# Optimization experiments

Measured on AMD Instinct MI355X. Metric: run time of the kernel, lower is better.

Reference implementation:

```python
import jax, jax.numpy as jnp
import numpy as np

B, NA, NB, DF, H, DO, NT = 32, 128, 1024, 128, 512, 128, 5
NPAIR = NT * NT  # nn_index = z1*5 + z2 -> 25 pair-type MLPs


def setup_inputs() -> dict:
    key = jax.random.key(0)
    ks = jax.random.split(key, 6)
    z = jax.random.randint(ks[0], (B, NA), 0, NT)
    r = jax.random.normal(ks[1], (B, NA, 3), jnp.float32) * 5.0
    x = jax.random.normal(ks[2], (B, NA, DF), jnp.float32)
    t = jax.random.randint(ks[3], (B, NB, 2), 0, NA)
    pad = NB // 8  # last 1/8 of bonds are -1 padding, as in the torch module
    t = t.at[:, NB - pad:, :].set(-1)
    # Stacked per-pair-type 2-layer MLP params (map_list)
    W1 = jax.random.normal(ks[4], (NPAIR, 2 * DF, H), jnp.float32) / np.sqrt(2.0 * DF)
    b1 = jnp.zeros((NPAIR, H), jnp.float32)
    W2 = jax.random.normal(ks[5], (NPAIR, H, DO), jnp.float32) / np.sqrt(1.0 * H)
    b2 = jnp.zeros((NPAIR, DO), jnp.float32)
    return dict(z=z, r=r, x=x, t=t, W1=W1, b1=b1, W2=W2, b2=b2)


def reference(z, r, x, t, W1, b1, W2, b2):
    n_batch, n_bonds, _ = t.shape
    n_atoms = x.shape[1]
    x_f = x.reshape(-1, x.shape[-1])          # [B*NA, DF]
    z_f = z.reshape(-1)                        # [B*NA]
    r_f = r.reshape(-1, 3)                     # [B*NA, 3]
    offs = (jnp.arange(n_batch) * n_atoms)[:, None, None]
    valid = t[:, :, 0] != -1                   # [B, NB]
    tg = jnp.clip(t, 0, None) + offs           # global atom indices (padding clamped to 0)
    t1 = tg[:, :, 0].reshape(-1)
    t2 = tg[:, :, 1].reshape(-1)
    vmask = valid.reshape(-1)                  # [N] = [B*NB]
    # gather+concat pair features; zero out padded rows (masked_scatter into zeros)
    x_c = jnp.concatenate([x_f[t1], x_f[t2]], axis=1) * vmask[:, None].astype(x.dtype)
    z1 = z_f[t1]
    z2 = z_f[t2]
    nn_index = jnp.where(vmask, z1 * NT + z2, -1)
    # per-pair-type MLP dispatch (loop over fixed 25 types; rows selected by mask)
    y = jnp.zeros((x_c.shape[0], W2.shape[-1]), x.dtype)
    for i in range(NPAIR):
        h = jax.nn.silu(x_c @ W1[i] + b1[i])
        out_i = h @ W2[i] + b2[i]
        y = jnp.where((nn_index == i)[:, None], out_i, y)
    y = y.reshape(n_batch, n_bonds, -1)
    # normalized bond vectors, zeroed for padded bonds
    v = (r_f[t2] - r_f[t1]).reshape(n_batch, n_bonds, 3)
    n2 = jnp.sum(v * v, axis=2, keepdims=True)
    v = v / jnp.sqrt(jnp.clip(n2, 1e-24, None))  # == clamp(norm, 1e-12)
    v = v * valid[:, :, None].astype(v.dtype)
    return (z, x, t, y, v)
```

## Files before the change

kernel.cpp:

```cpp
#include <hip/hip_runtime.h>
#include <cstddef>
#include <cstdint>

#define NBATCH 32
#define NATOM  128
#define DFEAT  128
#define HDIM   512
#define DOUT   128
#define NTYPE  5
#define NPAIR  25
#define NBOND  32768
#define CAP    1408
#define TPT    22
#define GBLK   550

#define OFF_X 4096
#define OFF_T 528384
#define OFF_Y 593920
#define OFF_V 4788224

#define PRE_A 580
#define PRE_B 256
#define PRE_C 1600
#define PRE_D 800
#define PRE_BLK (PRE_A+PRE_B+PRE_C+PRE_D)

typedef __attribute__((ext_vector_type(8))) short short8;
typedef __attribute__((ext_vector_type(4))) float f32x4;

#define GAS(x) ((__attribute__((address_space(1))) const void*)(x))
#define LAS(x) ((__attribute__((address_space(3))) void*)(x))

__device__ __forceinline__ unsigned short f2bf(float f) {
    unsigned u = __float_as_uint(f);
    u = (u + 0x7FFFu + ((u >> 16) & 1u)) >> 16;
    return (unsigned short)u;
}

__global__ __launch_bounds__(256) void k_pre(const int* __restrict__ z,
                                             const float* __restrict__ x,
                                             const int* __restrict__ t,
                                             const float* __restrict__ W1,
                                             const float* __restrict__ W2,
                                             float* __restrict__ out,
                                             short* __restrict__ x_bf,
                                             short* __restrict__ W1p,
                                             short* __restrict__ W2p,
                                             int* __restrict__ cursors) {
    int bid = blockIdx.x, tid = threadIdx.x;
    if (bid == 0 && tid < 32) cursors[tid] = 0;
    if (bid < PRE_A) {
        int i4 = (bid * 256 + tid) * 4;
        float4 o;
        if (i4 < OFF_X) {
            const int4 zi = *(const int4*)&z[i4];
            o = make_float4((float)zi.x, (float)zi.y, (float)zi.z, (float)zi.w);
        } else if (i4 < OFF_T) {
            o = *(const float4*)&x[i4 - OFF_X];
        } else {
            const int4 ti = *(const int4*)&t[i4 - OFF_T];
            o = make_float4((float)ti.x, (float)ti.y, (float)ti.z, (float)ti.w);
        }
        *(float4*)&out[i4] = o;
    } else if (bid < PRE_A + PRE_B) {
        int idx = (bid - PRE_A) * 256 + tid;
        const float4* px = (const float4*)&x[idx * 8];
        float4 fa = px[0], fb = px[1];
        short8 v;
        v[0]=(short)f2bf(fa.x); v[1]=(short)f2bf(fa.y); v[2]=(short)f2bf(fa.z); v[3]=(short)f2bf(fa.w);
        v[4]=(short)f2bf(fb.x); v[5]=(short)f2bf(fb.y); v[6]=(short)f2bf(fb.z); v[7]=(short)f2bf(fb.w);
        *((short8*)x_bf + idx) = v;
    } else if (bid < PRE_A + PRE_B + PRE_C) {
        int idx = (bid - PRE_A - PRE_B) * 256 + tid;
        int l  = idx & 63;
        int cf = (idx >> 6) & 31;
        int ks = (idx >> 11) & 7;
        int p  = idx >> 14;
        int col = cf*16 + (l & 15);
        int kb  = ks*32 + (l >> 4)*8;
        const float* src = W1 + ((size_t)p*2*DFEAT + kb)*HDIM + col;
        short8 v;
        #pragma unroll
        for (int j = 0; j < 8; ++j) v[j] = (short)f2bf(src[(size_t)j*HDIM]);
        *((short8*)W1p + idx) = v;
    } else {
        int idx = (bid - PRE_A - PRE_B - PRE_C) * 256 + tid;
        int l  = idx & 63;
        int cf = (idx >> 6) & 7;
        int ks = (idx >> 9) & 15;
        int p  = idx >> 13;
        int col = cf*16 + (l & 15);
        int kb  = ks*32 + (l >> 4)*8;
        const float* src = W2 + ((size_t)p*HDIM + kb)*DOUT + col;
        short8 v;
        #pragma unroll
        for (int j = 0; j < 8; ++j) v[j] = (short)f2bf(src[(size_t)j*DOUT]);
        *((short8*)W2p + idx) = v;
    }
}

__global__ __launch_bounds__(256) void k_scatter(const int* __restrict__ z,
                                                 const float* __restrict__ r,
                                                 const int* __restrict__ t,
                                                 float* __restrict__ out_v,
                                                 float* __restrict__ y_out,
                                                 int* __restrict__ cursors,
                                                 int* __restrict__ bond_ids) {
    __shared__ int hist[NPAIR];
    __shared__ int base[NPAIR];
    int tid = threadIdx.x;
    if (tid < NPAIR) hist[tid] = 0;
    __syncthreads();

    int i = blockIdx.x * 256 + tid;
    int b = i >> 10;
    int t1 = t[2*i], t2 = t[2*i+1];
    float vx = 0.f, vy = 0.f, vz = 0.f;
    int p = -1, rk = 0;
    if (t1 != -1) {
        int g1 = b*NATOM + t1, g2 = b*NATOM + t2;
        p = z[g1]*NTYPE + z[g2];
        rk = atomicAdd(&hist[p], 1);
        float dx = r[3*g2+0]-r[3*g1+0];
        float dy = r[3*g2+1]-r[3*g1+1];
        float dz = r[3*g2+2]-r[3*g1+2];
        float n2 = fmaxf(dx*dx+dy*dy+dz*dz, 1e-24f);
        float inv = 1.0f / sqrtf(n2);
        vx = dx*inv; vy = dy*inv; vz = dz*inv;
    } else {
        float4 zr = make_float4(0.f, 0.f, 0.f, 0.f);
        float4* yp = (float4*)&y_out[(size_t)i * DOUT];
        #pragma unroll
        for (int c = 0; c < DOUT/4; ++c) yp[c] = zr;
    }
    out_v[3*i+0] = vx; out_v[3*i+1] = vy; out_v[3*i+2] = vz;
    __syncthreads();
    if (tid < NPAIR) base[tid] = atomicAdd(&cursors[tid], hist[tid]);
    __syncthreads();
    if (p >= 0) {
        int pos = base[p] + rk;
        if (pos < CAP) bond_ids[p*CAP + pos] = i;
    }
}

#define STAGE(cc_, rr_) do { \
    int _c = (cc_), _r = (rr_); \
    if (_r >= 12) { _r -= 12; _c += 1; if (_c >= 4) _c = 0; } \
    const char* _s; \
    if (_r < 8) _s = (const char*)W1p + (((size_t)(p*8 + _r)*32 + _c*8 + wc*2)*64 + l)*16; \
    else        _s = (const char*)W2p + (((size_t)(p*16 + _c*4 + (_r-8))*8 + wc*2)*64 + l)*16; \
    char* _d = (char*)wbuf + ((rr_)%3)*8192 + wc*2048 + l*16; \
    __builtin_amdgcn_global_load_lds(GAS(_s), LAS(_d), 16, 0, 0); \
    __builtin_amdgcn_global_load_lds(GAS(_s+1024), LAS(_d+1024), 16, 0, 0); \
} while(0)

__global__ __launch_bounds__(256, 2) void k_gemm(const short* __restrict__ x_bf,
                                                 const int* __restrict__ t,
                                                 const short* __restrict__ W1p,
                                                 const float* __restrict__ b1,
                                                 const short* __restrict__ W2p,
                                                 const float* __restrict__ b2,
                                                 const int* __restrict__ cursors,
                                                 const int* __restrict__ bond_ids,
                                                 float* __restrict__ y_out) {
    int orig = blockIdx.x;
    int xcd = orig & 7, ib = orig >> 3;
    int wk = (xcd < 6 ? xcd*69 : 414 + (xcd-6)*68) + ib;
    int p = wk / TPT, tileIdx = wk % TPT;
    int cnt = min(cursors[p], CAP);
    if (tileIdx*64 >= cnt) return;
    int nb = min(64, cnt - tileIdx*64);
    int ntiles = (cnt + 63) >> 6;

    __shared__ short xs[64*256];
    __shared__ short hs[64*128];
    __shared__ char  wbuf[3*8192];
    __shared__ float b1s[HDIM];
    __shared__ float b2s[DOUT];
    __shared__ int   srow[64][2];
    __shared__ int   sb[64];

    int tid = threadIdx.x;
    int l = tid & 63, wc = tid >> 6;
    int lr = l & 15, lq = l >> 4;
    int klq = lq * 16;

    if (tid < 64) {
        int bi = (tid < nb) ? bond_ids[p*CAP + tileIdx*64 + tid] : -1;
        sb[tid] = bi;
        int r0 = 0, r1 = 0;
        if (bi >= 0) { int b = bi >> 10; r0 = b*NATOM + t[2*bi]; r1 = b*NATOM + t[2*bi+1]; }
        srow[tid][0] = r0; srow[tid][1] = r1;
    }

    {
        float snk = 0.f;
        const char* w1t = (const char*)W1p + (size_t)p*262144;
        int o1 = (int)(((long)tileIdx * 262144) / ntiles) & ~63;
        int e1 = (int)(((long)(tileIdx+1) * 262144) / ntiles);
        for (int o = o1 + tid*16; o < e1; o += 4096) {
            float4 v = *(const float4*)(w1t + o);
            snk += v.x + v.y + v.z + v.w;
        }
        const char* w2t = (const char*)W2p + (size_t)p*131072;
        int o2 = (int)(((long)tileIdx * 131072) / ntiles) & ~63;
        int e2 = (int)(((long)(tileIdx+1) * 131072) / ntiles);
        for (int o = o2 + tid*16; o < e2; o += 4096) {
            float4 v = *(const float4*)(w2t + o);
            snk += v.x + v.y + v.z + v.w;
        }
        asm volatile("" :: "v"(snk));
    }

    if (tid < 128)
        __builtin_amdgcn_global_load_lds(GAS((const char*)(b1 + (size_t)p*HDIM) + tid*16),
                                         LAS((char*)b1s + tid*16), 16, 0, 0);
    if (tid < 32)
        __builtin_amdgcn_global_load_lds(GAS((const char*)(b2 + (size_t)p*DOUT) + tid*16),
                                         LAS((char*)b2s + tid*16), 16, 0, 0);
    STAGE(0, 0);
    STAGE(0, 1);
    __syncthreads();

    #pragma unroll
    for (int j = 0; j < 8; ++j) {
        int o = j*4096 + tid*16;
        int row = o >> 9;
        int c16 = ((o >> 4) & 31) ^ (row & 7);
        const char* src = (const char*)x_bf + ((size_t)srow[row][c16 >> 4]*DFEAT + (c16 & 15)*8)*2;
        __builtin_amdgcn_global_load_lds(GAS(src), LAS((char*)xs + o), 16, 0, 0);
    }
    __syncthreads();

    f32x4 yacc[4][2] = {};

    for (int c = 0; c < 4; ++c) {
        float b1c0 = b1s[c*128 + wc*32 + lr];
        float b1c1 = b1s[c*128 + wc*32 + 16 + lr];
        f32x4 acc1[4][2] = {};
        #pragma unroll
        for (int r = 0; r < 8; ++r) {
            short8 a0, a1, a2, a3;
            {
                const char* xb = (const char*)xs;
                a0 = *(const short8*)(xb + (0*16+lr)*512 + ((r*64 + klq) ^ (((0*16+lr)&7) << 4)));
                a1 = *(const short8*)(xb + (1*16+lr)*512 + ((r*64 + klq) ^ (((1*16+lr)&7) << 4)));
                a2 = *(const short8*)(xb + (2*16+lr)*512 + ((r*64 + klq) ^ (((2*16+lr)&7) << 4)));
                a3 = *(const short8*)(xb + (3*16+lr)*512 + ((r*64 + klq) ^ (((3*16+lr)&7) << 4)));
            }
            STAGE(c, r + 2);
            asm volatile("s_waitcnt vmcnt(4)" ::: "memory");
            const char* wb = (const char*)wbuf + (r%3)*8192 + wc*2048 + l*16;
            short8 w0 = *(const short8*)wb;
            short8 w1 = *(const short8*)(wb + 1024);
            __builtin_amdgcn_s_setprio(1);
            acc1[0][0] = __builtin_amdgcn_mfma_f32_16x16x32_bf16(a0, w0, acc1[0][0], 0, 0, 0);
            acc1[0][1] = __builtin_amdgcn_mfma_f32_16x16x32_bf16(a0, w1, acc1[0][1], 0, 0, 0);
            acc1[1][0] = __builtin_amdgcn_mfma_f32_16x16x32_bf16(a1, w0, acc1[1][0], 0, 0, 0);
            acc1[1][1] = __builtin_amdgcn_mfma_f32_16x16x32_bf16(a1, w1, acc1[1][1], 0, 0, 0);
            acc1[2][0] = __builtin_amdgcn_mfma_f32_16x16x32_bf16(a2, w0, acc1[2][0], 0, 0, 0);
            acc1[2][1] = __builtin_amdgcn_mfma_f32_16x16x32_bf16(a2, w1, acc1[2][1], 0, 0, 0);
            acc1[3][0] = __builtin_amdgcn_mfma_f32_16x16x32_bf16(a3, w0, acc1[3][0], 0, 0, 0);
            acc1[3][1] = __builtin_amdgcn_mfma_f32_16x16x32_bf16(a3, w1, acc1[3][1], 0, 0, 0);
            __builtin_amdgcn_s_setprio(0);
        }
        #pragma unroll
        for (int rf = 0; rf < 4; ++rf) {
            #pragma unroll
            for (int cf = 0; cf < 2; ++cf) {
                int colb = (wc*32 + cf*16 + lr) * 2;
                float bb = cf ? b1c1 : b1c0;
                #pragma unroll
                for (int reg = 0; reg < 4; ++reg) {
                    int row = rf*16 + lq*4 + reg;
                    float sv = acc1[rf][cf][reg] + bb;
                    float hv = sv / (1.0f + __expf(-sv));
                    *(unsigned short*)((char*)hs + row*256 + (colb ^ ((row & 7) << 4))) = f2bf(hv);
                }
            }
        }
        asm volatile("s_waitcnt lgkmcnt(0)" ::: "memory");
        __builtin_amdgcn_s_barrier();

        #pragma unroll
        for (int r2 = 8; r2 < 12; ++r2) {
            short8 a0, a1, a2, a3;
            {
                const char* hb = (const char*)hs;
                int s2 = r2 - 8;
                a0 = *(const short8*)(hb + (0*16+lr)*256 + ((s2*64 + klq) ^ (((0*16+lr)&7) << 4)));
                a1 = *(const short8*)(hb + (1*16+lr)*256 + ((s2*64 + klq) ^ (((1*16+lr)&7) << 4)));
                a2 = *(const short8*)(hb + (2*16+lr)*256 + ((s2*64 + klq) ^ (((2*16+lr)&7) << 4)));
                a3 = *(const short8*)(hb + (3*16+lr)*256 + ((s2*64 + klq) ^ (((3*16+lr)&7) << 4)));
            }
            STAGE(c, r2 + 2);
            asm volatile("s_waitcnt vmcnt(4)" ::: "memory");
            const char* wb = (const char*)wbuf + (r2%3)*8192 + wc*2048 + l*16;
            short8 w0 = *(const short8*)wb;
            short8 w1 = *(const short8*)(wb + 1024);
            __builtin_amdgcn_s_setprio(1);
            yacc[0][0] = __builtin_amdgcn_mfma_f32_16x16x32_bf16(a0, w0, yacc[0][0], 0, 0, 0);
            yacc[0][1] = __builtin_amdgcn_mfma_f32_16x16x32_bf16(a0, w1, yacc[0][1], 0, 0, 0);
            yacc[1][0] = __builtin_amdgcn_mfma_f32_16x16x32_bf16(a1, w0, yacc[1][0], 0, 0, 0);
            yacc[1][1] = __builtin_amdgcn_mfma_f32_16x16x32_bf16(a1, w1, yacc[1][1], 0, 0, 0);
            yacc[2][0] = __builtin_amdgcn_mfma_f32_16x16x32_bf16(a2, w0, yacc[2][0], 0, 0, 0);
            yacc[2][1] = __builtin_amdgcn_mfma_f32_16x16x32_bf16(a2, w1, yacc[2][1], 0, 0, 0);
            yacc[3][0] = __builtin_amdgcn_mfma_f32_16x16x32_bf16(a3, w0, yacc[3][0], 0, 0, 0);
            yacc[3][1] = __builtin_amdgcn_mfma_f32_16x16x32_bf16(a3, w1, yacc[3][1], 0, 0, 0);
            __builtin_amdgcn_s_setprio(0);
        }
        if (c < 3) {
            asm volatile("s_waitcnt lgkmcnt(0)" ::: "memory");
            __builtin_amdgcn_s_barrier();
        }
    }

    float bo0 = b2s[wc*32 + lr], bo1 = b2s[wc*32 + 16 + lr];
    #pragma unroll
    for (int rf = 0; rf < 4; ++rf) {
        #pragma unroll
        for (int cf = 0; cf < 2; ++cf) {
            int col = wc*32 + cf*16 + lr;
            float bo = cf ? bo1 : bo0;
            #pragma unroll
            for (int reg = 0; reg < 4; ++reg) {
                int row = rf*16 + lq*4 + reg;
                if (row < nb)
                    y_out[(size_t)sb[row]*DOUT + col] = yacc[rf][cf][reg] + bo;
            }
        }
    }
}

extern "C" void kernel_launch(void* const* d_in, const int* in_sizes, int n_in,
                              void* d_out, int out_size, void* d_ws, size_t ws_size,
                              hipStream_t stream) {
    const int*   z  = (const int*)  d_in[0];
    const float* r  = (const float*)d_in[1];
    const float* x  = (const float*)d_in[2];
    const int*   t  = (const int*)  d_in[3];
    const float* W1 = (const float*)d_in[4];
    const float* b1 = (const float*)d_in[5];
    const float* W2 = (const float*)d_in[6];
    const float* b2 = (const float*)d_in[7];
    float* out = (float*)d_out;

    char* ws = (char*)d_ws;
    int*   cursors  = (int*)(ws);
    int*   bond_ids = (int*)(ws + 256);
    short* x_bf     = (short*)(ws + 141312);
    short* W1p      = (short*)(ws + 1189888);
    short* W2p      = (short*)(ws + 7743488);

    k_pre<<<PRE_BLK, 256, 0, stream>>>(z, x, t, W1, W2, out, x_bf, W1p, W2p, cursors);
    k_scatter<<<NBOND/256, 256, 0, stream>>>(z, r, t, out + OFF_V, out + OFF_Y, cursors, bond_ids);
    k_gemm<<<GBLK, 256, 0, stream>>>(x_bf, t, W1p, b1, W2p, b2, cursors, bond_ids, out + OFF_Y);
}
```

Measured before the change: 45.62 us.

## Merge scatter into prep kernel and software-pipeline GEMM fragment loads

Folds the bond scatter/histogram work into the preprocessing kernel, with cursors zeroed by a memset. This saves a kernel launch. The x→bf16 conversion now happens inside the copy branch, so x is read once. The GEMM inner loops prefetch the next step's LDS A and W fragments while the current MFMAs run, and wait on vmcnt(2) instead of vmcnt(4). SiLU uses v_rcp_f32 instead of a divide. The risks are higher register pressure, and a tighter vmcnt wait that may stall on the prefetch.

```diff
diff --git a/kernel.cpp b/kernel.cpp
--- a/kernel.cpp
+++ b/kernel.cpp
@@ -20,10 +20,10 @@
 #define OFF_V 4788224
 
 #define PRE_A 580
-#define PRE_B 256
 #define PRE_C 1600
 #define PRE_D 800
-#define PRE_BLK (PRE_A+PRE_B+PRE_C+PRE_D)
+#define SCAT  128
+#define PREP_BLK (PRE_A+PRE_C+PRE_D+SCAT)
 
 typedef __attribute__((ext_vector_type(8))) short short8;
 typedef __attribute__((ext_vector_type(4))) float f32x4;
@@ -37,18 +37,19 @@
     return (unsigned short)u;
 }
 
-__global__ __launch_bounds__(256) void k_pre(const int* __restrict__ z,
-                                             const float* __restrict__ x,
-                                             const int* __restrict__ t,
-                                             const float* __restrict__ W1,
-                                             const float* __restrict__ W2,
-                                             float* __restrict__ out,
-                                             short* __restrict__ x_bf,
-                                             short* __restrict__ W1p,
-                                             short* __restrict__ W2p,
-                                             int* __restrict__ cursors) {
+__global__ __launch_bounds__(256) void k_prep(const int* __restrict__ z,
+                                              const float* __restrict__ x,
+                                              const int* __restrict__ t,
+                                              const float* __restrict__ r,
+                                              const float* __restrict__ W1,
+                                              const float* __restrict__ W2,
+                                              float* __restrict__ out,
+                                              short* __restrict__ x_bf,
+                                              short* __restrict__ W1p,
+                                              short* __restrict__ W2p,
+                                              int* __restrict__ cursors,
+                                              int* __restrict__ bond_ids) {
     int bid = blockIdx.x, tid = threadIdx.x;
-    if (bid == 0 && tid < 32) cursors[tid] = 0;
     if (bid < PRE_A) {
         int i4 = (bid * 256 + tid) * 4;
         float4 o;
@@ -57,21 +58,17 @@
             o = make_float4((float)zi.x, (float)zi.y, (float)zi.z, (float)zi.w);
         } else if (i4 < OFF_T) {
             o = *(const float4*)&x[i4 - OFF_X];
+            short4 s4;
+            s4.x = (short)f2bf(o.x); s4.y = (short)f2bf(o.y);
+            s4.z = (short)f2bf(o.z); s4.w = (short)f2bf(o.w);
+            *(short4*)&x_bf[i4 - OFF_X] = s4;
         } else {
             const int4 ti = *(const int4*)&t[i4 - OFF_T];
             o = make_float4((float)ti.x, (float)ti.y, (float)ti.z, (float)ti.w);
         }
         *(float4*)&out[i4] = o;
-    } else if (bid < PRE_A + PRE_B) {
+    } else if (bid < PRE_A + PRE_C) {
         int idx = (bid - PRE_A) * 256 + tid;
-        const float4* px = (const float4*)&x[idx * 8];
-        float4 fa = px[0], fb = px[1];
-        short8 v;
-        v[0]=(short)f2bf(fa.x); v[1]=(short)f2bf(fa.y); v[2]=(short)f2bf(fa.z); v[3]=(short)f2bf(fa.w);
-        v[4]=(short)f2bf(fb.x); v[5]=(short)f2bf(fb.y); v[6]=(short)f2bf(fb.z); v[7]=(short)f2bf(fb.w);
-        *((short8*)x_bf + idx) = v;
-    } else if (bid < PRE_A + PRE_B + PRE_C) {
-        int idx = (bid - PRE_A - PRE_B) * 256 + tid;
         int l  = idx & 63;
         int cf = (idx >> 6) & 31;
         int ks = (idx >> 11) & 7;
@@ -83,8 +80,8 @@
         #pragma unroll
         for (int j = 0; j < 8; ++j) v[j] = (short)f2bf(src[(size_t)j*HDIM]);
         *((short8*)W1p + idx) = v;
-    } else {
-        int idx = (bid - PRE_A - PRE_B - PRE_C) * 256 + tid;
+    } else if (bid < PRE_A + PRE_C + PRE_D) {
+        int idx = (bid - PRE_A - PRE_C) * 256 + tid;
         int l  = idx & 63;
         int cf = (idx >> 6) & 7;
         int ks = (idx >> 9) & 15;
@@ -96,50 +93,41 @@
         #pragma unroll
         for (int j = 0; j < 8; ++j) v[j] = (short)f2bf(src[(size_t)j*DOUT]);
         *((short8*)W2p + idx) = v;
-    }
-}
-
-__global__ __launch_bounds__(256) void k_scatter(const int* __restrict__ z,
-                                                 const float* __restrict__ r,
-                                                 const int* __restrict__ t,
-                                                 float* __restrict__ out_v,
-                                                 float* __restrict__ y_out,
-                                                 int* __restrict__ cursors,
-                                                 int* __restrict__ bond_ids) {
-    __shared__ int hist[NPAIR];
-    __shared__ int base[NPAIR];
-    int tid = threadIdx.x;
-    if (tid < NPAIR) hist[tid] = 0;
-    __syncthreads();
-
-    int i = blockIdx.x * 256 + tid;
-    int b = i >> 10;
-    int t1 = t[2*i], t2 = t[2*i+1];
-    float vx = 0.f, vy = 0.f, vz = 0.f;
-    int p = -1, rk = 0;
-    if (t1 != -1) {
-        int g1 = b*NATOM + t1, g2 = b*NATOM + t2;
-        p = z[g1]*NTYPE + z[g2];
-        rk = atomicAdd(&hist[p], 1);
-        float dx = r[3*g2+0]-r[3*g1+0];
-        float dy = r[3*g2+1]-r[3*g1+1];
-        float dz = r[3*g2+2]-r[3*g1+2];
-        float n2 = fmaxf(dx*dx+dy*dy+dz*dz, 1e-24f);
-        float inv = 1.0f / sqrtf(n2);
-        vx = dx*inv; vy = dy*inv; vz = dz*inv;
     } else {
-        float4 zr = make_float4(0.f, 0.f, 0.f, 0.f);
-        float4* yp = (float4*)&y_out[(size_t)i * DOUT];
-        #pragma unroll
-        for (int c = 0; c < DOUT/4; ++c) yp[c] = zr;
-    }
-    out_v[3*i+0] = vx; out_v[3*i+1] = vy; out_v[3*i+2] = vz;
-    __syncthreads();
-    if (tid < NPAIR) base[tid] = atomicAdd(&cursors[tid], hist[tid]);
-    __syncthreads();
-    if (p >= 0) {
-        int pos = base[p] + rk;
-        if (pos < CAP) bond_ids[p*CAP + pos] = i;
+        __shared__ int hist[NPAIR];
+        __shared__ int base[NPAIR];
+        if (tid < NPAIR) hist[tid] = 0;
+        __syncthreads();
+        int i = (bid - PRE_A - PRE_C - PRE_D) * 256 + tid;
+        int b = i >> 10;
+        int t1 = t[2*i], t2 = t[2*i+1];
+        float vx = 0.f, vy = 0.f, vz = 0.f;
+        int p = -1, rk = 0;
+        if (t1 != -1) {
+            int g1 = b*NATOM + t1, g2 = b*NATOM + t2;
+            p = z[g1]*NTYPE + z[g2];
+            rk = atomicAdd(&hist[p], 1);
+            float dx = r[3*g2+0]-r[3*g1+0];
+            float dy = r[3*g2+1]-r[3*g1+1];
+            float dz = r[3*g2+2]-r[3*g1+2];
+            float n2 = fmaxf(dx*dx+dy*dy+dz*dz, 1e-24f);
+            float inv = 1.0f / sqrtf(n2);
+            vx = dx*inv; vy = dy*inv; vz = dz*inv;
+        } else {
+            float4 zr = make_float4(0.f, 0.f, 0.f, 0.f);
+            float4* yp = (float4*)&out[OFF_Y + (size_t)i * DOUT];
+            #pragma unroll
+            for (int c = 0; c < DOUT/4; ++c) yp[c] = zr;
+        }
+        float* out_v = out + OFF_V;
+        out_v[3*i+0] = vx; out_v[3*i+1] = vy; out_v[3*i+2] = vz;
+        __syncthreads();
+        if (tid < NPAIR) base[tid] = atomicAdd(&cursors[tid], hist[tid]);
+        __syncthreads();
+        if (p >= 0) {
+            int pos = base[p] + rk;
+            if (pos < CAP) bond_ids[p*CAP + pos] = i;
+        }
     }
 }
 
@@ -152,6 +140,28 @@
     char* _d = (char*)wbuf + ((rr_)%3)*8192 + wc*2048 + l*16; \
     __builtin_amdgcn_global_load_lds(GAS(_s), LAS(_d), 16, 0, 0); \
     __builtin_amdgcn_global_load_lds(GAS(_s+1024), LAS(_d+1024), 16, 0, 0); \
+} while(0)
+
+#define XFRAG(dst, rf_, step_) do { \
+    int _row = (rf_)*16 + lr; \
+    dst = *(const short8*)((const char*)xs + _row*512 + (((step_)*64 + klq) ^ ((_row & 7) << 4))); \
+} while(0)
+#define HFRAG(dst, rf_, step_) do { \
+    int _row = (rf_)*16 + lr; \
+    dst = *(const short8*)((const char*)hs + _row*256 + (((step_)*64 + klq) ^ ((_row & 7) << 4))); \
+} while(0)
+
+#define MFMA8(ACC) do { \
+    __builtin_amdgcn_s_setprio(1); \
+    ACC[0][0] = __builtin_amdgcn_mfma_f32_16x16x32_bf16(a0, w0, ACC[0][0], 0, 0, 0); \
+    ACC[0][1] = __builtin_amdgcn_mfma_f32_16x16x32_bf16(a0, w1, ACC[0][1], 0, 0, 0); \
+    ACC[1][0] = __builtin_amdgcn_mfma_f32_16x16x32_bf16(a1, w0, ACC[1][0], 0, 0, 0); \
+    ACC[1][1] = __builtin_amdgcn_mfma_f32_16x16x32_bf16(a1, w1, ACC[1][1], 0, 0, 0); \
+    ACC[2][0] = __builtin_amdgcn_mfma_f32_16x16x32_bf16(a2, w0, ACC[2][0], 0, 0, 0); \
+    ACC[2][1] = __builtin_amdgcn_mfma_f32_16x16x32_bf16(a2, w1, ACC[2][1], 0, 0, 0); \
+    ACC[3][0] = __builtin_amdgcn_mfma_f32_16x16x32_bf16(a3, w0, ACC[3][0], 0, 0, 0); \
+    ACC[3][1] = __builtin_amdgcn_mfma_f32_16x16x32_bf16(a3, w1, ACC[3][1], 0, 0, 0); \
+    __builtin_amdgcn_s_setprio(0); \
 } while(0)
 
 __global__ __launch_bounds__(256, 2) void k_gemm(const short* __restrict__ x_bf,
@@ -234,35 +244,30 @@
 
     f32x4 yacc[4][2] = {};
 
+    short8 a0, a1, a2, a3, w0, w1;
+    XFRAG(a0, 0, 0); XFRAG(a1, 1, 0); XFRAG(a2, 2, 0); XFRAG(a3, 3, 0);
+    {
+        const char* wb = (const char*)wbuf + wc*2048 + l*16;
+        w0 = *(const short8*)wb;
+        w1 = *(const short8*)(wb + 1024);
+    }
+
     for (int c = 0; c < 4; ++c) {
         float b1c0 = b1s[c*128 + wc*32 + lr];
         float b1c1 = b1s[c*128 + wc*32 + 16 + lr];
         f32x4 acc1[4][2] = {};
         #pragma unroll
-        for (int r = 0; r < 8; ++r) {
-            short8 a0, a1, a2, a3;
-            {
-                const char* xb = (const char*)xs;
-                a0 = *(const short8*)(xb + (0*16+lr)*512 + ((r*64 + klq) ^ (((0*16+lr)&7) << 4)));
-                a1 = *(const short8*)(xb + (1*16+lr)*512 + ((r*64 + klq) ^ (((1*16+lr)&7) << 4)));
-                a2 = *(const short8*)(xb + (2*16+lr)*512 + ((r*64 + klq) ^ (((2*16+lr)&7) << 4)));
-                a3 = *(const short8*)(xb + (3*16+lr)*512 + ((r*64 + klq) ^ (((3*16+lr)&7) << 4)));
-            }
-            STAGE(c, r + 2);
-            asm volatile("s_waitcnt vmcnt(4)" ::: "memory");
-            const char* wb = (const char*)wbuf + (r%3)*8192 + wc*2048 + l*16;
-            short8 w0 = *(const short8*)wb;
-            short8 w1 = *(const short8*)(wb + 1024);
-            __builtin_amdgcn_s_setprio(1);
-            acc1[0][0] = __builtin_amdgcn_mfma_f32_16x16x32_bf16(a0, w0, acc1[0][0], 0, 0, 0);
-            acc1[0][1] = __builtin_amdgcn_mfma_f32_16x16x32_bf16(a0, w1, acc1[0][1], 0, 0, 0);
-            acc1[1][0] = __builtin_amdgcn_mfma_f32_16x16x32_bf16(a1, w0, acc1[1][0], 0, 0, 0);
-            acc1[1][1] = __builtin_amdgcn_mfma_f32_16x16x32_bf16(a1, w1, acc1[1][1], 0, 0, 0);
-            acc1[2][0] = __builtin_amdgcn_mfma_f32_16x16x32_bf16(a2, w0, acc1[2][0], 0, 0, 0);
-            acc1[2][1] = __builtin_amdgcn_mfma_f32_16x16x32_bf16(a2, w1, acc1[2][1], 0, 0, 0);
-            acc1[3][0] = __builtin_amdgcn_mfma_f32_16x16x32_bf16(a3, w0, acc1[3][0], 0, 0, 0);
-            acc1[3][1] = __builtin_amdgcn_mfma_f32_16x16x32_bf16(a3, w1, acc1[3][1], 0, 0, 0);
-            __builtin_amdgcn_s_setprio(0);
+        for (int rr = 0; rr < 8; ++rr) {
+            short8 na0, na1, na2, na3;
+            if (rr < 7) { XFRAG(na0, 0, rr+1); XFRAG(na1, 1, rr+1); XFRAG(na2, 2, rr+1); XFRAG(na3, 3, rr+1); }
+            STAGE(c, rr + 2);
+            asm volatile("s_waitcnt vmcnt(2)" ::: "memory");
+            const char* nwb = (const char*)wbuf + ((rr+1)%3)*8192 + wc*2048 + l*16;
+            short8 nw0 = *(const short8*)nwb;
+            short8 nw1 = *(const short8*)(nwb + 1024);
+            MFMA8(acc1);
+            if (rr < 7) { a0 = na0; a1 = na1; a2 = na2; a3 = na3; }
+            w0 = nw0; w1 = nw1;
         }
         #pragma unroll
         for (int rf = 0; rf < 4; ++rf) {
@@ -274,40 +279,30 @@
                 for (int reg = 0; reg < 4; ++reg) {
                     int row = rf*16 + lq*4 + reg;
                     float sv = acc1[rf][cf][reg] + bb;
-                    float hv = sv / (1.0f + __expf(-sv));
-                    *(unsigned short*)((char*)hs + row*256 + (colb ^ ((row & 7) << 4))) = f2bf(hv);
+                    float den = 1.0f + __expf(-sv);
+                    float rc;
+                    asm("v_rcp_f32 %0, %1" : "=v"(rc) : "v"(den));
+                    *(unsigned short*)((char*)hs + row*256 + (colb ^ ((row & 7) << 4))) = f2bf(sv * rc);
                 }
             }
         }
         asm volatile("s_waitcnt lgkmcnt(0)" ::: "memory");
         __builtin_amdgcn_s_barrier();
 
-        #pragma unroll
-        for (int r2 = 8; r2 < 12; ++r2) {
-            short8 a0, a1, a2, a3;
-            {
-                const char* hb = (const char*)hs;
-                int s2 = r2 - 8;
-                a0 = *(const short8*)(hb + (0*16+lr)*256 + ((s2*64 + klq) ^ (((0*16+lr)&7) << 4)));
-                a1 = *(const short8*)(hb + (1*16+lr)*256 + ((s2*64 + klq) ^ (((1*16+lr)&7) << 4)));
-                a2 = *(const short8*)(hb + (2*16+lr)*256 + ((s2*64 + klq) ^ (((2*16+lr)&7) << 4)));
-                a3 = *(const short8*)(hb + (3*16+lr)*256 + ((s2*64 + klq) ^ (((3*16+lr)&7) << 4)));
-            }
-            STAGE(c, r2 + 2);
-            asm volatile("s_waitcnt vmcnt(4)" ::: "memory");
-            const char* wb = (const char*)wbuf + (r2%3)*8192 + wc*2048 + l*16;
-            short8 w0 = *(const short8*)wb;
-            short8 w1 = *(const short8*)(wb + 1024);
-            __builtin_amdgcn_s_setprio(1);
-            yacc[0][0] = __builtin_amdgcn_mfma_f32_16x16x32_bf16(a0, w0, yacc[0][0], 0, 0, 0);
-            yacc[0][1] = __builtin_amdgcn_mfma_f32_16x16x32_bf16(a0, w1, yacc[0][1], 0, 0, 0);
-            yacc[1][0] = __builtin_amdgcn_mfma_f32_16x16x32_bf16(a1, w0, yacc[1][0], 0, 0, 0);
-            yacc[1][1] = __builtin_amdgcn_mfma_f32_16x16x32_bf16(a1, w1, yacc[1][1], 0, 0, 0);
-            yacc[2][0] = __builtin_amdgcn_mfma_f32_16x16x32_bf16(a2, w0, yacc[2][0], 0, 0, 0);
-            yacc[2][1] = __builtin_amdgcn_mfma_f32_16x16x32_bf16(a2, w1, yacc[2][1], 0, 0, 0);
-            yacc[3][0] = __builtin_amdgcn_mfma_f32_16x16x32_bf16(a3, w0, yacc[3][0], 0, 0, 0);
-            yacc[3][1] = __builtin_amdgcn_mfma_f32_16x16x32_bf16(a3, w1, yacc[3][1], 0, 0, 0);
-            __builtin_amdgcn_s_setprio(0);
+        HFRAG(a0, 0, 0); HFRAG(a1, 1, 0); HFRAG(a2, 2, 0); HFRAG(a3, 3, 0);
+        #pragma unroll
+        for (int r2 = 0; r2 < 4; ++r2) {
+            short8 na0, na1, na2, na3;
+            if (r2 < 3) { HFRAG(na0, 0, r2+1); HFRAG(na1, 1, r2+1); HFRAG(na2, 2, r2+1); HFRAG(na3, 3, r2+1); }
+            else        { XFRAG(na0, 0, 0);    XFRAG(na1, 1, 0);    XFRAG(na2, 2, 0);    XFRAG(na3, 3, 0);    }
+            STAGE(c, r2 + 10);
+            asm volatile("s_waitcnt vmcnt(2)" ::: "memory");
+            const char* nwb = (const char*)wbuf + ((r2+9)%3)*8192 + wc*2048 + l*16;
+            short8 nw0 = *(const short8*)nwb;
+            short8 nw1 = *(const short8*)(nwb + 1024);
+            MFMA8(yacc);
+            a0 = na0; a1 = na1; a2 = na2; a3 = na3;
+            w0 = nw0; w1 = nw1;
         }
         if (c < 3) {
             asm volatile("s_waitcnt lgkmcnt(0)" ::: "memory");
@@ -352,7 +347,7 @@
     short* W1p      = (short*)(ws + 1189888);
     short* W2p      = (short*)(ws + 7743488);
 
-    k_pre<<<PRE_BLK, 256, 0, stream>>>(z, x, t, W1, W2, out, x_bf, W1p, W2p, cursors);
-    k_scatter<<<NBOND/256, 256, 0, stream>>>(z, r, t, out + OFF_V, out + OFF_Y, cursors, bond_ids);
+    hipMemsetAsync(cursors, 0, 128, stream);
+    k_prep<<<PREP_BLK, 256, 0, stream>>>(z, x, t, r, W1, W2, out, x_bf, W1p, W2p, cursors, bond_ids);
     k_gemm<<<GBLK, 256, 0, stream>>>(x_bf, t, W1p, b1, W2p, b2, cursors, bond_ids, out + OFF_Y);
 }
```

Result: slower. 48.67 us (+6.7%).

## Fuse scatter into prep kernel and interleave W1/W2 packing per stage

Applied to the files above, without the earlier changes.

Merges the bond-scatter kernel into the preprocessing kernel, with cursor reset done by a memset, and folds the x bf16 conversion into the output-copy blocks. It packs W1 and W2 into one stage-ordered buffer so each GEMM stage loads a contiguous 8KB chunk, and gathers x rows directly from bond_ids without the srow staging barrier. It also removes setprio hints and uses a fast reciprocal in SiLU. The aim is to cut launch count, address arithmetic and one sync, at the cost of an extra memset and a larger prep kernel in which scatter blocks run alongside packing blocks.

```diff
diff --git a/kernel.cpp b/kernel.cpp
--- a/kernel.cpp
+++ b/kernel.cpp
@@ -20,10 +20,9 @@
 #define OFF_V 4788224
 
 #define PRE_A 580
-#define PRE_B 256
-#define PRE_C 1600
-#define PRE_D 800
-#define PRE_BLK (PRE_A+PRE_B+PRE_C+PRE_D)
+#define PACKB 2400
+#define SCAT  128
+#define PRE_BLK (PRE_A+PACKB+SCAT)
 
 typedef __attribute__((ext_vector_type(8))) short short8;
 typedef __attribute__((ext_vector_type(4))) float f32x4;
@@ -40,15 +39,15 @@
 __global__ __launch_bounds__(256) void k_pre(const int* __restrict__ z,
                                              const float* __restrict__ x,
                                              const int* __restrict__ t,
+                                             const float* __restrict__ r,
                                              const float* __restrict__ W1,
                                              const float* __restrict__ W2,
                                              float* __restrict__ out,
                                              short* __restrict__ x_bf,
-                                             short* __restrict__ W1p,
-                                             short* __restrict__ W2p,
-                                             int* __restrict__ cursors) {
+                                             short* __restrict__ Wpk,
+                                             int* __restrict__ cursors,
+                                             int* __restrict__ bond_ids) {
     int bid = blockIdx.x, tid = threadIdx.x;
-    if (bid == 0 && tid < 32) cursors[tid] = 0;
     if (bid < PRE_A) {
         int i4 = (bid * 256 + tid) * 4;
         float4 o;
@@ -57,108 +56,90 @@
             o = make_float4((float)zi.x, (float)zi.y, (float)zi.z, (float)zi.w);
         } else if (i4 < OFF_T) {
             o = *(const float4*)&x[i4 - OFF_X];
+            short4 s4;
+            s4.x = (short)f2bf(o.x); s4.y = (short)f2bf(o.y);
+            s4.z = (short)f2bf(o.z); s4.w = (short)f2bf(o.w);
+            *(short4*)&x_bf[i4 - OFF_X] = s4;
         } else {
             const int4 ti = *(const int4*)&t[i4 - OFF_T];
             o = make_float4((float)ti.x, (float)ti.y, (float)ti.z, (float)ti.w);
         }
         *(float4*)&out[i4] = o;
-    } else if (bid < PRE_A + PRE_B) {
+    } else if (bid < PRE_A + PACKB) {
         int idx = (bid - PRE_A) * 256 + tid;
-        const float4* px = (const float4*)&x[idx * 8];
-        float4 fa = px[0], fb = px[1];
+        int l   = idx & 63;
+        int u   = (idx >> 6) & 1;
+        int wcp = (idx >> 7) & 3;
+        int q   = idx >> 9;
+        int p   = q / 48;
+        int s   = q - p*48;
+        int c   = s / 12;
+        int rr  = s - c*12;
+        int lr = l & 15, kb = (l >> 4)*8;
         short8 v;
-        v[0]=(short)f2bf(fa.x); v[1]=(short)f2bf(fa.y); v[2]=(short)f2bf(fa.z); v[3]=(short)f2bf(fa.w);
-        v[4]=(short)f2bf(fb.x); v[5]=(short)f2bf(fb.y); v[6]=(short)f2bf(fb.z); v[7]=(short)f2bf(fb.w);
-        *((short8*)x_bf + idx) = v;
-    } else if (bid < PRE_A + PRE_B + PRE_C) {
-        int idx = (bid - PRE_A - PRE_B) * 256 + tid;
-        int l  = idx & 63;
-        int cf = (idx >> 6) & 31;
-        int ks = (idx >> 11) & 7;
-        int p  = idx >> 14;
-        int col = cf*16 + (l & 15);
-        int kb  = ks*32 + (l >> 4)*8;
-        const float* src = W1 + ((size_t)p*2*DFEAT + kb)*HDIM + col;
-        short8 v;
-        #pragma unroll
-        for (int j = 0; j < 8; ++j) v[j] = (short)f2bf(src[(size_t)j*HDIM]);
-        *((short8*)W1p + idx) = v;
+        if (rr < 8) {
+            int col = (c*8 + wcp*2 + u)*16 + lr;
+            const float* src = W1 + ((size_t)p*256 + rr*32 + kb)*HDIM + col;
+            #pragma unroll
+            for (int j = 0; j < 8; ++j) v[j] = (short)f2bf(src[(size_t)j*HDIM]);
+        } else {
+            int col = (wcp*2 + u)*16 + lr;
+            const float* src = W2 + ((size_t)p*HDIM + (c*4 + (rr-8))*32 + kb)*DOUT + col;
+            #pragma unroll
+            for (int j = 0; j < 8; ++j) v[j] = (short)f2bf(src[(size_t)j*DOUT]);
+        }
+        *((short8*)Wpk + idx) = v;
     } else {
-        int idx = (bid - PRE_A - PRE_B - PRE_C) * 256 + tid;
-        int l  = idx & 63;
-        int cf = (idx >> 6) & 7;
-        int ks = (idx >> 9) & 15;
-        int p  = idx >> 13;
-        int col = cf*16 + (l & 15);
-        int kb  = ks*32 + (l >> 4)*8;
-        const float* src = W2 + ((size_t)p*HDIM + kb)*DOUT + col;
-        short8 v;
-        #pragma unroll
-        for (int j = 0; j < 8; ++j) v[j] = (short)f2bf(src[(size_t)j*DOUT]);
-        *((short8*)W2p + idx) = v;
+        __shared__ int hist[NPAIR];
+        __shared__ int base[NPAIR];
+        if (tid < NPAIR) hist[tid] = 0;
+        __syncthreads();
+        int i = (bid - PRE_A - PACKB) * 256 + tid;
+        int b = i >> 10;
+        int t1 = t[2*i], t2 = t[2*i+1];
+        float vx = 0.f, vy = 0.f, vz = 0.f;
+        int p = -1, rk = 0;
+        if (t1 != -1) {
+            int g1 = b*NATOM + t1, g2 = b*NATOM + t2;
+            p = z[g1]*NTYPE + z[g2];
+            rk = atomicAdd(&hist[p], 1);
+            float dx = r[3*g2+0]-r[3*g1+0];
+            float dy = r[3*g2+1]-r[3*g1+1];
+            float dz = r[3*g2+2]-r[3*g1+2];
+            float n2 = fmaxf(dx*dx+dy*dy+dz*dz, 1e-24f);
+            float inv = 1.0f / sqrtf(n2);
+            vx = dx*inv; vy = dy*inv; vz = dz*inv;
+        } else {
+            float4 zr = make_float4(0.f, 0.f, 0.f, 0.f);
+            float4* yp = (float4*)&out[OFF_Y + (size_t)i * DOUT];
+            #pragma unroll
+            for (int c2 = 0; c2 < DOUT/4; ++c2) yp[c2] = zr;
+        }
+        float* out_v = out + OFF_V;
+        out_v[3*i+0] = vx; out_v[3*i+1] = vy; out_v[3*i+2] = vz;
+        __syncthreads();
+        if (tid < NPAIR) base[tid] = atomicAdd(&cursors[tid], hist[tid]);
+        __syncthreads();
+        if (p >= 0) {
+            int pos = base[p] + rk;
+            if (pos < CAP) bond_ids[p*CAP + pos] = i;
+        }
     }
 }
 
-__global__ __launch_bounds__(256) void k_scatter(const int* __restrict__ z,
-                                                 const float* __restrict__ r,
-                                                 const int* __restrict__ t,
-                                                 float* __restrict__ out_v,
-                                                 float* __restrict__ y_out,
-                                                 int* __restrict__ cursors,
-                                                 int* __restrict__ bond_ids) {
-    __shared__ int hist[NPAIR];
-    __shared__ int base[NPAIR];
-    int tid = threadIdx.x;
-    if (tid < NPAIR) hist[tid] = 0;
-    __syncthreads();
-
-    int i = blockIdx.x * 256 + tid;
-    int b = i >> 10;
-    int t1 = t[2*i], t2 = t[2*i+1];
-    float vx = 0.f, vy = 0.f, vz = 0.f;
-    int p = -1, rk = 0;
-    if (t1 != -1) {
-        int g1 = b*NATOM + t1, g2 = b*NATOM + t2;
-        p = z[g1]*NTYPE + z[g2];
-        rk = atomicAdd(&hist[p], 1);
-        float dx = r[3*g2+0]-r[3*g1+0];
-        float dy = r[3*g2+1]-r[3*g1+1];
-        float dz = r[3*g2+2]-r[3*g1+2];
-        float n2 = fmaxf(dx*dx+dy*dy+dz*dz, 1e-24f);
-        float inv = 1.0f / sqrtf(n2);
-        vx = dx*inv; vy = dy*inv; vz = dz*inv;
-    } else {
-        float4 zr = make_float4(0.f, 0.f, 0.f, 0.f);
-        float4* yp = (float4*)&y_out[(size_t)i * DOUT];
-        #pragma unroll
-        for (int c = 0; c < DOUT/4; ++c) yp[c] = zr;
-    }
-    out_v[3*i+0] = vx; out_v[3*i+1] = vy; out_v[3*i+2] = vz;
-    __syncthreads();
-    if (tid < NPAIR) base[tid] = atomicAdd(&cursors[tid], hist[tid]);
-    __syncthreads();
-    if (p >= 0) {
-        int pos = base[p] + rk;
-        if (pos < CAP) bond_ids[p*CAP + pos] = i;
-    }
-}
-
-#define STAGE(cc_, rr_) do { \
-    int _c = (cc_), _r = (rr_); \
-    if (_r >= 12) { _r -= 12; _c += 1; if (_c >= 4) _c = 0; } \
-    const char* _s; \
-    if (_r < 8) _s = (const char*)W1p + (((size_t)(p*8 + _r)*32 + _c*8 + wc*2)*64 + l)*16; \
-    else        _s = (const char*)W2p + (((size_t)(p*16 + _c*4 + (_r-8))*8 + wc*2)*64 + l)*16; \
-    char* _d = (char*)wbuf + ((rr_)%3)*8192 + wc*2048 + l*16; \
-    __builtin_amdgcn_global_load_lds(GAS(_s), LAS(_d), 16, 0, 0); \
-    __builtin_amdgcn_global_load_lds(GAS(_s+1024), LAS(_d+1024), 16, 0, 0); \
+#define STAGE(ss_) do { \
+    int _ss = (ss_); \
+    int _sw = (_ss >= 48) ? _ss - 48 : _ss; \
+    const char* _src = wkbase + (size_t)_sw * 8192; \
+    char* _d = wbbase + (_ss % 3) * 8192; \
+    __builtin_amdgcn_global_load_lds(GAS(_src), LAS(_d), 16, 0, 0); \
+    __builtin_amdgcn_global_load_lds(GAS(_src+1024), LAS(_d+1024), 16, 0, 0); \
 } while(0)
 
 __global__ __launch_bounds__(256, 2) void k_gemm(const short* __restrict__ x_bf,
                                                  const int* __restrict__ t,
-                                                 const short* __restrict__ W1p,
+                                                 const short* __restrict__ Wpk,
                                                  const float* __restrict__ b1,
-                                                 const short* __restrict__ W2p,
                                                  const float* __restrict__ b2,
                                                  const int* __restrict__ cursors,
                                                  const int* __restrict__ bond_ids,
@@ -177,7 +158,6 @@
     __shared__ char  wbuf[3*8192];
     __shared__ float b1s[HDIM];
     __shared__ float b2s[DOUT];
-    __shared__ int   srow[64][2];
     __shared__ int   sb[64];
 
     int tid = threadIdx.x;
@@ -185,28 +165,33 @@
     int lr = l & 15, lq = l >> 4;
     int klq = lq * 16;
 
-    if (tid < 64) {
-        int bi = (tid < nb) ? bond_ids[p*CAP + tileIdx*64 + tid] : -1;
-        sb[tid] = bi;
-        int r0 = 0, r1 = 0;
-        if (bi >= 0) { int b = bi >> 10; r0 = b*NATOM + t[2*bi]; r1 = b*NATOM + t[2*bi+1]; }
-        srow[tid][0] = r0; srow[tid][1] = r1;
+    const char* wkbase = (const char*)Wpk + ((size_t)(p*48)*4 + wc)*2048 + l*16;
+    char* wbbase = (char*)wbuf + wc*2048 + l*16;
+
+    if (tid < 64)
+        sb[tid] = (tid < nb) ? bond_ids[p*CAP + tileIdx*64 + tid] : -1;
+
+    #pragma unroll
+    for (int j = 0; j < 8; ++j) {
+        int o = j*4096 + tid*16;
+        int row = o >> 9;
+        int c16 = ((o >> 4) & 31) ^ (row & 7);
+        int atom = 0;
+        if (row < nb) {
+            int bi = bond_ids[p*CAP + tileIdx*64 + row];
+            atom = (bi >> 10)*NATOM + t[2*bi + (c16 >> 4)];
+        }
+        const char* src = (const char*)x_bf + ((size_t)atom*DFEAT + (c16 & 15)*8)*2;
+        __builtin_amdgcn_global_load_lds(GAS(src), LAS((char*)xs + o), 16, 0, 0);
     }
 
     {
         float snk = 0.f;
-        const char* w1t = (const char*)W1p + (size_t)p*262144;
-        int o1 = (int)(((long)tileIdx * 262144) / ntiles) & ~63;
-        int e1 = (int)(((long)(tileIdx+1) * 262144) / ntiles);
+        const char* wkt = (const char*)Wpk + (size_t)p*393216;
+        int o1 = (int)(((long)tileIdx * 393216) / ntiles) & ~63;
+        int e1 = (int)(((long)(tileIdx+1) * 393216) / ntiles);
         for (int o = o1 + tid*16; o < e1; o += 4096) {
-            float4 v = *(const float4*)(w1t + o);
-            snk += v.x + v.y + v.z + v.w;
-        }
-        const char* w2t = (const char*)W2p + (size_t)p*131072;
-        int o2 = (int)(((long)tileIdx * 131072) / ntiles) & ~63;
-        int e2 = (int)(((long)(tileIdx+1) * 131072) / ntiles);
-        for (int o = o2 + tid*16; o < e2; o += 4096) {
-            float4 v = *(const float4*)(w2t + o);
+            float4 v = *(const float4*)(wkt + o);
             snk += v.x + v.y + v.z + v.w;
         }
         asm volatile("" :: "v"(snk));
@@ -218,18 +203,8 @@
     if (tid < 32)
         __builtin_amdgcn_global_load_lds(GAS((const char*)(b2 + (size_t)p*DOUT) + tid*16),
                                          LAS((char*)b2s + tid*16), 16, 0, 0);
-    STAGE(0, 0);
-    STAGE(0, 1);
-    __syncthreads();
-
-    #pragma unroll
-    for (int j = 0; j < 8; ++j) {
-        int o = j*4096 + tid*16;
-        int row = o >> 9;
-        int c16 = ((o >> 4) & 31) ^ (row & 7);
-        const char* src = (const char*)x_bf + ((size_t)srow[row][c16 >> 4]*DFEAT + (c16 & 15)*8)*2;
-        __builtin_amdgcn_global_load_lds(GAS(src), LAS((char*)xs + o), 16, 0, 0);
-    }
+    STAGE(0);
+    STAGE(1);
     __syncthreads();
 
     f32x4 yacc[4][2] = {};
@@ -239,21 +214,21 @@
         float b1c1 = b1s[c*128 + wc*32 + 16 + lr];
         f32x4 acc1[4][2] = {};
         #pragma unroll
-        for (int r = 0; r < 8; ++r) {
+        for (int rr = 0; rr < 8; ++rr) {
+            int s = c*12 + rr;
             short8 a0, a1, a2, a3;
             {
                 const char* xb = (const char*)xs;
-                a0 = *(const short8*)(xb + (0*16+lr)*512 + ((r*64 + klq) ^ (((0*16+lr)&7) << 4)));
-                a1 = *(const short8*)(xb + (1*16+lr)*512 + ((r*64 + klq) ^ (((1*16+lr)&7) << 4)));
-                a2 = *(const short8*)(xb + (2*16+lr)*512 + ((r*64 + klq) ^ (((2*16+lr)&7) << 4)));
-                a3 = *(const short8*)(xb + (3*16+lr)*512 + ((r*64 + klq) ^ (((3*16+lr)&7) << 4)));
+                a0 = *(const short8*)(xb + (0*16+lr)*512 + ((rr*64 + klq) ^ (((0*16+lr)&7) << 4)));
+                a1 = *(const short8*)(xb + (1*16+lr)*512 + ((rr*64 + klq) ^ (((1*16+lr)&7) << 4)));
+                a2 = *(const short8*)(xb + (2*16+lr)*512 + ((rr*64 + klq) ^ (((2*16+lr)&7) << 4)));
+                a3 = *(const short8*)(xb + (3*16+lr)*512 + ((rr*64 + klq) ^ (((3*16+lr)&7) << 4)));
             }
-            STAGE(c, r + 2);
+            STAGE(s + 2);
             asm volatile("s_waitcnt vmcnt(4)" ::: "memory");
-            const char* wb = (const char*)wbuf + (r%3)*8192 + wc*2048 + l*16;
+            const char* wb = wbbase + (rr % 3) * 8192;
             short8 w0 = *(const short8*)wb;
             short8 w1 = *(const short8*)(wb + 1024);
-            __builtin_amdgcn_s_setprio(1);
             acc1[0][0] = __builtin_amdgcn_mfma_f32_16x16x32_bf16(a0, w0, acc1[0][0], 0, 0, 0);
             acc1[0][1] = __builtin_amdgcn_mfma_f32_16x16x32_bf16(a0, w1, acc1[0][1], 0, 0, 0);
             acc1[1][0] = __builtin_amdgcn_mfma_f32_16x16x32_bf16(a1, w0, acc1[1][0], 0, 0, 0);
@@ -262,7 +237,6 @@
             acc1[2][1] = __builtin_amdgcn_mfma_f32_16x16x32_bf16(a2, w1, acc1[2][1], 0, 0, 0);
             acc1[3][0] = __builtin_amdgcn_mfma_f32_16x16x32_bf16(a3, w0, acc1[3][0], 0, 0, 0);
             acc1[3][1] = __builtin_amdgcn_mfma_f32_16x16x32_bf16(a3, w1, acc1[3][1], 0, 0, 0);
-            __builtin_amdgcn_s_setprio(0);
         }
         #pragma unroll
         for (int rf = 0; rf < 4; ++rf) {
@@ -274,7 +248,7 @@
                 for (int reg = 0; reg < 4; ++reg) {
                     int row = rf*16 + lq*4 + reg;
                     float sv = acc1[rf][cf][reg] + bb;
-                    float hv = sv / (1.0f + __expf(-sv));
+                    float hv = sv * __builtin_amdgcn_rcpf(1.0f + __expf(-sv));
                     *(unsigned short*)((char*)hs + row*256 + (colb ^ ((row & 7) << 4))) = f2bf(hv);
                 }
             }
@@ -283,22 +257,21 @@
         __builtin_amdgcn_s_barrier();
 
         #pragma unroll
-        for (int r2 = 8; r2 < 12; ++r2) {
+        for (int r2 = 0; r2 < 4; ++r2) {
+            int s = c*12 + 8 + r2;
             short8 a0, a1, a2, a3;
             {
                 const char* hb = (const char*)hs;
-                int s2 = r2 - 8;
-                a0 = *(const short8*)(hb + (0*16+lr)*256 + ((s2*64 + klq) ^ (((0*16+lr)&7) << 4)));
-                a1 = *(const short8*)(hb + (1*16+lr)*256 + ((s2*64 + klq) ^ (((1*16+lr)&7) << 4)));
-                a2 = *(const short8*)(hb + (2*16+lr)*256 + ((s2*64 + klq) ^ (((2*16+lr)&7) << 4)));
-                a3 = *(const short8*)(hb + (3*16+lr)*256 + ((s2*64 + klq) ^ (((3*16+lr)&7) << 4)));
+                a0 = *(const short8*)(hb + (0*16+lr)*256 + ((r2*64 + klq) ^ (((0*16+lr)&7) << 4)));
+                a1 = *(const short8*)(hb + (1*16+lr)*256 + ((r2*64 + klq) ^ (((1*16+lr)&7) << 4)));
+                a2 = *(const short8*)(hb + (2*16+lr)*256 + ((r2*64 + klq) ^ (((2*16+lr)&7) << 4)));
+                a3 = *(const short8*)(hb + (3*16+lr)*256 + ((r2*64 + klq) ^ (((3*16+lr)&7) << 4)));
             }
-            STAGE(c, r2 + 2);
+            STAGE(s + 2);
             asm volatile("s_waitcnt vmcnt(4)" ::: "memory");
-            const char* wb = (const char*)wbuf + (r2%3)*8192 + wc*2048 + l*16;
+            const char* wb = wbbase + ((8 + r2) % 3) * 8192;
             short8 w0 = *(const short8*)wb;
             short8 w1 = *(const short8*)(wb + 1024);
-            __builtin_amdgcn_s_setprio(1);
             yacc[0][0] = __builtin_amdgcn_mfma_f32_16x16x32_bf16(a0, w0, yacc[0][0], 0, 0, 0);
             yacc[0][1] = __builtin_amdgcn_mfma_f32_16x16x32_bf16(a0, w1, yacc[0][1], 0, 0, 0);
             yacc[1][0] = __builtin_amdgcn_mfma_f32_16x16x32_bf16(a1, w0, yacc[1][0], 0, 0, 0);
@@ -307,13 +280,13 @@
             yacc[2][1] = __builtin_amdgcn_mfma_f32_16x16x32_bf16(a2, w1, yacc[2][1], 0, 0, 0);
             yacc[3][0] = __builtin_amdgcn_mfma_f32_16x16x32_bf16(a3, w0, yacc[3][0], 0, 0, 0);
             yacc[3][1] = __builtin_amdgcn_mfma_f32_16x16x32_bf16(a3, w1, yacc[3][1], 0, 0, 0);
-            __builtin_amdgcn_s_setprio(0);
         }
         if (c < 3) {
             asm volatile("s_waitcnt lgkmcnt(0)" ::: "memory");
             __builtin_amdgcn_s_barrier();
         }
     }
+    asm volatile("s_waitcnt vmcnt(0)" ::: "memory");
 
     float bo0 = b2s[wc*32 + lr], bo1 = b2s[wc*32 + 16 + lr];
     #pragma unroll
@@ -349,10 +322,9 @@
     int*   cursors  = (int*)(ws);
     int*   bond_ids = (int*)(ws + 256);
     short* x_bf     = (short*)(ws + 141312);
-    short* W1p      = (short*)(ws + 1189888);
-    short* W2p      = (short*)(ws + 7743488);
-
-    k_pre<<<PRE_BLK, 256, 0, stream>>>(z, x, t, W1, W2, out, x_bf, W1p, W2p, cursors);
-    k_scatter<<<NBOND/256, 256, 0, stream>>>(z, r, t, out + OFF_V, out + OFF_Y, cursors, bond_ids);
-    k_gemm<<<GBLK, 256, 0, stream>>>(x_bf, t, W1p, b1, W2p, b2, cursors, bond_ids, out + OFF_Y);
+    short* Wpk      = (short*)(ws + 1189888);
+
+    hipMemsetAsync(cursors, 0, 128, stream);
+    k_pre<<<PRE_BLK, 256, 0, stream>>>(z, x, t, r, W1, W2, out, x_bf, Wpk, cursors, bond_ids);
+    k_gemm<<<GBLK, 256, 0, stream>>>(x_bf, t, Wpk, b1, b2, cursors, bond_ids, out + OFF_Y);
 }
```

Result: slower. 50.08 us (+9.8%).
